# Kernel optimization log

Measured on AMD Instinct MI355X. Metric: run time of the kernel, lower is better.

Reference implementation:

```python
import jax, jax.numpy as jnp
import numpy as np

NEG = -999999.0

def setup_inputs() -> dict:
    key = jax.random.key(0)
    ks = jax.random.split(key, 8)
    B, N, H, D = 8, 2048, 1, 256  # in_dim = H*D = 256
    in_dim = H * D
    feat_in = jax.random.normal(ks[0], (B, N, in_dim), dtype=jnp.float32)
    adj = jax.random.randint(ks[1], (B, N, N), 0, 2, dtype=jnp.int32)
    # parameters (xavier-ish scales)
    W  = jax.random.normal(ks[2], (H, in_dim, D), dtype=jnp.float32) * (2.0 / (in_dim + D)) ** 0.5
    b  = jnp.zeros((D,), dtype=jnp.float32)
    Ws = jax.random.normal(ks[3], (1, 2 * D), dtype=jnp.float32) * (2.0 / (2 * D + 1)) ** 0.5  # strengh.weight
    bs = jnp.zeros((1,), dtype=jnp.float32)                                                     # strengh.bias
    Hw = jax.random.normal(ks[4], (in_dim, in_dim), dtype=jnp.float32) * (1.0 / in_dim) ** 0.5  # H.weight
    Hb = jnp.zeros((in_dim,), dtype=jnp.float32)                                                # H.bias
    return {"feat_in": feat_in, "adj": adj, "W": W, "b": b, "Ws": Ws, "bs": bs, "Hw": Hw, "Hb": Hb}

def reference(feat_in, adj, W, b, Ws, bs, Hw, Hb):
    B, N, in_dim = feat_in.shape
    H, _, D = W.shape
    h = jnp.einsum('bni,hid->bhnd', feat_in, W)                    # [B,H,N,D]
    # strengh(cat(h_src, h_dst)) decomposed: H_src[b,i,j]=h[b,i], H_dst[b,i,j]=h[b,j]
    ws_src, ws_dst = Ws[0, :D], Ws[0, D:]
    a_src = jnp.einsum('bhnd,d->bhn', h, ws_src)                   # per row i
    a_dst = jnp.einsum('bhnd,d->bhn', h, ws_dst)                   # per col j
    attn = jax.nn.sigmoid(a_src[:, :, :, None] + a_dst[:, :, None, :] + bs[0])  # [B,H,N,N]
    strict_low = jnp.tril(jnp.ones((N, N), dtype=feat_in.dtype), -1)
    attn = attn * strict_low                                        # zero outside strict lower triangle
    I_A = jnp.eye(N, dtype=feat_in.dtype) - attn                    # [B,H,N,N]
    I_A_raw = I_A
    # allowed positions: lower triangle (incl diag) AND adj==1
    low = jnp.tril(jnp.ones((N, N), dtype=jnp.bool_), 0)
    allowed = low[None, None] & (adj[:, None] == 1)                 # [B,H,N,N]
    scores = jnp.where(allowed, I_A, NEG)
    P = jax.nn.softmax(scores, axis=-1)
    feat_out = jnp.einsum('bhij,bhjd->bhid', P, h) + b              # [B,H,N,D]
    feat_out = feat_out.transpose(0, 2, 1, 3).reshape(B, N, H * D)
    feat_out = jax.nn.elu(feat_out)
    gate = jax.nn.sigmoid(feat_in @ Hw.T + Hb)
    out = gate * feat_out + (1.0 - gate) * feat_in                  # dropout = identity (eval)
    return out, I_A_raw
```

## Files before the change

kernel.cpp:

```cpp
#include <hip/hip_runtime.h>
#include <math.h>

constexpr int Bc = 8, Nc = 2048, Dc = 256;
constexpr int BN = Bc * Nc;

typedef __attribute__((ext_vector_type(8))) short short8;
typedef __attribute__((ext_vector_type(4))) float f32x4;

__device__ __forceinline__ float sigmoidf_(float x) { return 1.0f / (1.0f + expf(-x)); }

__device__ __forceinline__ unsigned short f2bf(float f) {
    unsigned int u = __float_as_uint(f);
    u = (u + 0x7FFFu + ((u >> 16) & 1u)) >> 16;
    return (unsigned short)u;
}

__device__ __forceinline__ short8 ld_frag(const unsigned short* base) {
    ushort4 lo = *(const ushort4*)(base);
    ushort4 hi = *(const ushort4*)(base + 16);
    short8 a;
    a[0] = (short)lo.x; a[1] = (short)lo.y; a[2] = (short)lo.z; a[3] = (short)lo.w;
    a[4] = (short)hi.x; a[5] = (short)hi.y; a[6] = (short)hi.z; a[7] = (short)hi.w;
    return a;
}

__device__ __forceinline__ f32x4 fz4() { f32x4 z = {0.f, 0.f, 0.f, 0.f}; return z; }

__global__ __launch_bounds__(256) void cast_kernel(const float* __restrict__ f,
                                                   unsigned short* __restrict__ o) {
    int i = (blockIdx.x * 256 + threadIdx.x) * 4;
    float4 v = *(const float4*)(f + i);
    ushort4 u = {f2bf(v.x), f2bf(v.y), f2bf(v.z), f2bf(v.w)};
    *(ushort4*)(o + i) = u;
}

__global__ __launch_bounds__(256) void pack_bt_kernel(const float* __restrict__ W,
                                                      const float* __restrict__ Hw,
                                                      unsigned short* __restrict__ BmT) {
    int idx = blockIdx.x * 256 + threadIdx.x;
    int o = idx >> 8, k = idx & 255;
    float v = (o < 256) ? W[k * 256 + o] : Hw[(o - 256) * 256 + k];
    BmT[idx] = f2bf(v);
}

__global__ __launch_bounds__(256) void gemm_mfma(const unsigned short* __restrict__ featb,
                                                 const unsigned short* __restrict__ BmT,
                                                 const float* __restrict__ Hb,
                                                 float* __restrict__ h,
                                                 float* __restrict__ gate) {
    const int tid = threadIdx.x, lane = tid & 63, w = tid >> 6;
    const int g16 = lane >> 4, li = lane & 15;
    const int m0 = blockIdx.x * 64, nw = blockIdx.y * 128 + w * 32;
    f32x4 acc[4][2];
#pragma unroll
    for (int rf = 0; rf < 4; ++rf)
#pragma unroll
        for (int cf = 0; cf < 2; ++cf) acc[rf][cf] = fz4();
    for (int k0 = 0; k0 < 256; k0 += 32) {
        short8 Af[4];
#pragma unroll
        for (int rf = 0; rf < 4; ++rf)
            Af[rf] = ld_frag(featb + (size_t)(m0 + rf * 16 + li) * 256 + k0 + g16 * 4);
#pragma unroll
        for (int cf = 0; cf < 2; ++cf) {
            short8 Bf = ld_frag(BmT + (size_t)(nw + cf * 16 + li) * 256 + k0 + g16 * 4);
#pragma unroll
            for (int rf = 0; rf < 4; ++rf)
                acc[rf][cf] = __builtin_amdgcn_mfma_f32_16x16x32_bf16(Af[rf], Bf, acc[rf][cf], 0, 0, 0);
        }
    }
#pragma unroll
    for (int rf = 0; rf < 4; ++rf)
#pragma unroll
        for (int cf = 0; cf < 2; ++cf) {
            const int n = nw + cf * 16 + li;
#pragma unroll
            for (int reg = 0; reg < 4; ++reg) {
                const int m = m0 + rf * 16 + g16 * 4 + reg;
                float v = acc[rf][cf][reg];
                if (n < 256) h[(size_t)m * 256 + n] = v;
                else gate[(size_t)m * 256 + (n - 256)] = sigmoidf_(v + Hb[n - 256]);
            }
        }
}

__global__ __launch_bounds__(256) void tr64_kernel(const float* __restrict__ h,
                                                   unsigned short* __restrict__ hT) {
    __shared__ float tile[64][65];
    const int j0 = blockIdx.x * 64, d0 = blockIdx.y * 64, b = blockIdx.z;
    const int tid = threadIdx.x;
#pragma unroll
    for (int p = 0; p < 16; ++p) {
        int idx = tid + p * 256;
        int jl = idx >> 6, dl = idx & 63;
        tile[jl][dl] = h[((size_t)b * Nc + j0 + jl) * 256 + d0 + dl];
    }
    __syncthreads();
#pragma unroll
    for (int p = 0; p < 16; ++p) {
        int idx = tid + p * 256;
        int dl = idx >> 6, jl = idx & 63;
        hT[((size_t)b * 256 + d0 + dl) * Nc + j0 + jl] = f2bf(tile[jl][dl]);
    }
}

__global__ __launch_bounds__(256) void asrc_kernel(const float* __restrict__ h,
                                                   const float* __restrict__ Ws,
                                                   float* __restrict__ a_src,
                                                   float* __restrict__ a_dst) {
    const int row = blockIdx.x * 4 + (threadIdx.x >> 6);
    const int lane = threadIdx.x & 63;
    float4 h4 = ((const float4*)(h + (size_t)row * 256))[lane];
    float4 ws = ((const float4*)Ws)[lane];
    float4 wd = ((const float4*)(Ws + 256))[lane];
    float s1 = h4.x * ws.x + h4.y * ws.y + h4.z * ws.z + h4.w * ws.w;
    float s2 = h4.x * wd.x + h4.y * wd.y + h4.z * wd.z + h4.w * wd.w;
#pragma unroll
    for (int m = 32; m >= 1; m >>= 1) {
        s1 += __shfl_xor(s1, m, 64);
        s2 += __shfl_xor(s2, m, 64);
    }
    if (lane == 0) { a_src[row] = s1; a_dst[row] = s2; }
}

__global__ __launch_bounds__(256) void mean_kernel(const float* __restrict__ h,
                                                   float* __restrict__ mean_h) {
    const int blk = blockIdx.x;
    const int b = blk >> 5, part = blk & 31;
    const int d = threadIdx.x;
    float sum = 0.f;
    const float* base = h + ((size_t)b * Nc + part * 64) * 256 + d;
#pragma unroll 4
    for (int r = 0; r < 64; ++r) sum += base[(size_t)r * 256];
    atomicAdd(&mean_h[b * 256 + d], sum);
}

constexpr int CHUNK = 8;
__global__ __launch_bounds__(256) void score_mfma(
    const int* __restrict__ adj, const unsigned short* __restrict__ hT,
    const float* __restrict__ a_src, const float* __restrict__ a_dst,
    const float* __restrict__ bs_p, float* __restrict__ out2,
    float* __restrict__ accO, float* __restrict__ sArr) {
    __shared__ unsigned short pt[32][40];
    __shared__ float sh_as[32];

    const int bid = blockIdx.x;
    const int b = bid & 7;
    int t = bid >> 3;
    int g = 0;
    while (g < 7 && 4 * (g + 1) * (g + 2) <= t) ++g;
    const int r_ = t - 4 * g * (g + 1);
    const int ib = g * 8 + r_ / (g + 1);
    const int c = r_ % (g + 1);
    const int i0 = ib * 32;
    const int t0 = c * CHUNK;
    const int t1 = min(ib + 1, t0 + CHUNK);

    const int tid = threadIdx.x;
    const int lane = tid & 63;
    const int w = tid >> 6;
    const int g16 = lane >> 4, li = lane & 15;
    const int jj_ = tid & 31;
    const int r0 = tid >> 5;
    const float bsv = bs_p[0];

    if (tid < 32) sh_as[tid] = a_src[b * Nc + i0 + tid];
    __syncthreads();

    f32x4 acc[2][4];
#pragma unroll
    for (int rf = 0; rf < 2; ++rf)
#pragma unroll
        for (int cf = 0; cf < 4; ++cf) acc[rf][cf] = fz4();
    f32x4 sacc0 = fz4(), sacc1 = fz4();
    short8 ones;
#pragma unroll
    for (int e = 0; e < 8; ++e) ones[e] = (short)0x3F80;

    const unsigned short* hTb = hT + (size_t)b * 256 * Nc;

    for (int tt = t0; tt < t1; ++tt) {
        const int j0 = tt * 32;
        if (tt > t0) __syncthreads();
        {
            const int j = j0 + jj_;
            const float adstj = a_dst[b * Nc + j];
#pragma unroll
            for (int q = 0; q < 4; ++q) {
                const int r = r0 + 8 * q;
                const int i = i0 + r;
                const int av = adj[((size_t)b * Nc + i) * Nc + j];
                float IA, p;
                if (j > i) { IA = 0.f; p = 0.f; }
                else {
                    IA = (j == i) ? 1.f : -sigmoidf_(sh_as[r] + adstj + bsv);
                    out2[((size_t)b * Nc + i) * Nc + j] = IA;
                    p = (av == 1) ? expf(IA - 1.f) : 0.f;
                }
                pt[r][jj_] = f2bf(p);
            }
        }
        __syncthreads();
        {
            short8 A0 = ld_frag(&pt[li][g16 * 4]);
            short8 A1 = ld_frag(&pt[16 + li][g16 * 4]);
            if (w == 0) {
                sacc0 = __builtin_amdgcn_mfma_f32_16x16x32_bf16(A0, ones, sacc0, 0, 0, 0);
                sacc1 = __builtin_amdgcn_mfma_f32_16x16x32_bf16(A1, ones, sacc1, 0, 0, 0);
            }
#pragma unroll
            for (int cf = 0; cf < 4; ++cf) {
                const unsigned short* bp =
                    hTb + (size_t)(w * 64 + cf * 16 + li) * Nc + j0 + g16 * 4;
                short8 Bf = ld_frag(bp);
                acc[0][cf] = __builtin_amdgcn_mfma_f32_16x16x32_bf16(A0, Bf, acc[0][cf], 0, 0, 0);
                acc[1][cf] = __builtin_amdgcn_mfma_f32_16x16x32_bf16(A1, Bf, acc[1][cf], 0, 0, 0);
            }
        }
    }
#pragma unroll
    for (int rf = 0; rf < 2; ++rf)
#pragma unroll
        for (int cf = 0; cf < 4; ++cf) {
            const int row = i0 + rf * 16 + g16 * 4;
            float* dst = accO + ((size_t)b * Nc + row) * 256 + w * 64 + cf * 16 + li;
#pragma unroll
            for (int reg = 0; reg < 4; ++reg)
                atomicAdd(dst + (size_t)reg * 256, acc[rf][cf][reg]);
        }
    if (w == 0 && li == 0) {
#pragma unroll
        for (int reg = 0; reg < 4; ++reg) {
            atomicAdd(&sArr[b * Nc + i0 + g16 * 4 + reg], sacc0[reg]);
            atomicAdd(&sArr[b * Nc + i0 + 16 + g16 * 4 + reg], sacc1[reg]);
        }
    }
}

__global__ __launch_bounds__(256) void epilogue_kernel(
    const float* __restrict__ gate, const float* __restrict__ feat,
    const float* __restrict__ bvec, const float* __restrict__ mean_h,
    const float* __restrict__ sArr, float* __restrict__ out1) {
    const int row = blockIdx.x * 4 + (threadIdx.x >> 6);
    const int lane = threadIdx.x & 63;
    const int b = row >> 11;
    const size_t g = (size_t)row * 256;
    const float s = sArr[row];
    float4 v;
    if (s == 0.f) {
        float4 mh = ((const float4*)(mean_h + b * 256))[lane];
        const float inv = 1.0f / Nc;
        v.x = mh.x * inv; v.y = mh.y * inv; v.z = mh.z * inv; v.w = mh.w * inv;
    } else {
        float4 a = ((const float4*)(out1 + g))[lane];
        const float inv = 1.0f / s;
        v.x = a.x * inv; v.y = a.y * inv; v.z = a.z * inv; v.w = a.w * inv;
    }
    const float4 b4 = ((const float4*)bvec)[lane];
    v.x += b4.x; v.y += b4.y; v.z += b4.z; v.w += b4.w;
    v.x = v.x > 0.f ? v.x : expf(v.x) - 1.f;
    v.y = v.y > 0.f ? v.y : expf(v.y) - 1.f;
    v.z = v.z > 0.f ? v.z : expf(v.z) - 1.f;
    v.w = v.w > 0.f ? v.w : expf(v.w) - 1.f;
    const float4 g4 = ((const float4*)(gate + g))[lane];
    const float4 f4 = ((const float4*)(feat + g))[lane];
    float4 o;
    o.x = g4.x * v.x + (1.f - g4.x) * f4.x;
    o.y = g4.y * v.y + (1.f - g4.y) * f4.y;
    o.z = g4.z * v.z + (1.f - g4.z) * f4.z;
    o.w = g4.w * v.w + (1.f - g4.w) * f4.w;
    ((float4*)(out1 + g))[lane] = o;
}

extern "C" void kernel_launch(void* const* d_in, const int* in_sizes, int n_in,
                              void* d_out, int out_size, void* d_ws, size_t ws_size,
                              hipStream_t stream) {
    const float* feat = (const float*)d_in[0];
    const int* adj = (const int*)d_in[1];
    const float* W = (const float*)d_in[2];
    const float* bvec = (const float*)d_in[3];
    const float* Ws = (const float*)d_in[4];
    const float* bs = (const float*)d_in[5];
    const float* Hw = (const float*)d_in[6];
    const float* Hb = (const float*)d_in[7];

    float* ws = (float*)d_ws;
    unsigned short* featb = (unsigned short*)ws;
    unsigned short* hT = featb;
    unsigned short* BmT = featb + 4194304;
    float* h = ws + 2097152 + 65536;
    float* gate = h + 4194304;
    float* a_src = gate + 4194304;
    float* a_dst = a_src + 16384;
    float* mean_h = a_dst + 16384;
    float* sArr = mean_h + 2048;

    float* out1 = (float*)d_out;
    float* out2 = out1 + (size_t)BN * 256;

    hipLaunchKernelGGL(cast_kernel, dim3(4096), dim3(256), 0, stream, feat, featb);
    hipLaunchKernelGGL(pack_bt_kernel, dim3(512), dim3(256), 0, stream, W, Hw, BmT);
    hipLaunchKernelGGL(gemm_mfma, dim3(256, 4), dim3(256), 0, stream, featb, BmT, Hb, h, gate);
    hipLaunchKernelGGL(tr64_kernel, dim3(32, 4, 8), dim3(256), 0, stream, h, hT);
    hipLaunchKernelGGL(asrc_kernel, dim3(4096), dim3(256), 0, stream, h, Ws, a_src, a_dst);
    hipMemsetAsync(mean_h, 0, 2048 * sizeof(float), stream);
    hipLaunchKernelGGL(mean_kernel, dim3(256), dim3(256), 0, stream, h, mean_h);
    hipMemsetAsync(sArr, 0, (size_t)BN * sizeof(float), stream);
    hipMemsetAsync(out1, 0, (size_t)BN * 256 * sizeof(float), stream);
    hipMemsetAsync(out2, 0, (size_t)BN * (size_t)Nc * sizeof(float), stream);
    hipLaunchKernelGGL(score_mfma, dim3(2304), dim3(256), 0, stream,
                       adj, hT, a_src, a_dst, bs, out2, out1, sArr);
    hipLaunchKernelGGL(epilogue_kernel, dim3(4096), dim3(256), 0, stream,
                       gate, feat, bvec, mean_h, sArr, out1);
}
```

Before: 454.8 us.

## Fuse score, normalization and epilogue into one per-row-block kernel

After: 494.5 us. 1.09x slower.

```diff
diff --git a/kernel.cpp b/kernel.cpp
--- a/kernel.cpp
+++ b/kernel.cpp
@@ -13,6 +13,9 @@
     unsigned int u = __float_as_uint(f);
     u = (u + 0x7FFFu + ((u >> 16) & 1u)) >> 16;
     return (unsigned short)u;
+}
+__device__ __forceinline__ float bf2f(unsigned short s) {
+    return __uint_as_float(((unsigned int)s) << 16);
 }
 
 __device__ __forceinline__ short8 ld_frag(const unsigned short* base) {
@@ -23,7 +26,6 @@
     a[4] = (short)hi.x; a[5] = (short)hi.y; a[6] = (short)hi.z; a[7] = (short)hi.w;
     return a;
 }
-
 __device__ __forceinline__ f32x4 fz4() { f32x4 z = {0.f, 0.f, 0.f, 0.f}; return z; }
 
 __global__ __launch_bounds__(256) void cast_kernel(const float* __restrict__ f,
@@ -84,8 +86,12 @@
         }
 }
 
-__global__ __launch_bounds__(256) void tr64_kernel(const float* __restrict__ h,
-                                                   unsigned short* __restrict__ hT) {
+__global__ __launch_bounds__(256) void tr64f_kernel(const float* __restrict__ h,
+                                                    const float* __restrict__ Ws,
+                                                    unsigned short* __restrict__ hT,
+                                                    float* __restrict__ a_src,
+                                                    float* __restrict__ a_dst,
+                                                    float* __restrict__ mean_h) {
     __shared__ float tile[64][65];
     const int j0 = blockIdx.x * 64, d0 = blockIdx.y * 64, b = blockIdx.z;
     const int tid = threadIdx.x;
@@ -102,174 +108,176 @@
         int dl = idx >> 6, jl = idx & 63;
         hT[((size_t)b * 256 + d0 + dl) * Nc + j0 + jl] = f2bf(tile[jl][dl]);
     }
-}
-
-__global__ __launch_bounds__(256) void asrc_kernel(const float* __restrict__ h,
-                                                   const float* __restrict__ Ws,
-                                                   float* __restrict__ a_src,
-                                                   float* __restrict__ a_dst) {
-    const int row = blockIdx.x * 4 + (threadIdx.x >> 6);
-    const int lane = threadIdx.x & 63;
-    float4 h4 = ((const float4*)(h + (size_t)row * 256))[lane];
-    float4 ws = ((const float4*)Ws)[lane];
-    float4 wd = ((const float4*)(Ws + 256))[lane];
-    float s1 = h4.x * ws.x + h4.y * ws.y + h4.z * ws.z + h4.w * ws.w;
-    float s2 = h4.x * wd.x + h4.y * wd.y + h4.z * wd.z + h4.w * wd.w;
-#pragma unroll
-    for (int m = 32; m >= 1; m >>= 1) {
-        s1 += __shfl_xor(s1, m, 64);
-        s2 += __shfl_xor(s2, m, 64);
-    }
-    if (lane == 0) { a_src[row] = s1; a_dst[row] = s2; }
-}
-
-__global__ __launch_bounds__(256) void mean_kernel(const float* __restrict__ h,
-                                                   float* __restrict__ mean_h) {
-    const int blk = blockIdx.x;
-    const int b = blk >> 5, part = blk & 31;
-    const int d = threadIdx.x;
-    float sum = 0.f;
-    const float* base = h + ((size_t)b * Nc + part * 64) * 256 + d;
-#pragma unroll 4
-    for (int r = 0; r < 64; ++r) sum += base[(size_t)r * 256];
-    atomicAdd(&mean_h[b * 256 + d], sum);
-}
-
-constexpr int CHUNK = 8;
-__global__ __launch_bounds__(256) void score_mfma(
+    {
+        const int jl = tid >> 2, q = tid & 3;
+        float s1 = 0.f, s2 = 0.f;
+#pragma unroll
+        for (int e = 0; e < 16; ++e) {
+            const float hv = tile[jl][q * 16 + e];
+            s1 = fmaf(hv, Ws[d0 + q * 16 + e], s1);
+            s2 = fmaf(hv, Ws[256 + d0 + q * 16 + e], s2);
+        }
+        s1 += __shfl_xor(s1, 1); s1 += __shfl_xor(s1, 2);
+        s2 += __shfl_xor(s2, 1); s2 += __shfl_xor(s2, 2);
+        if (q == 0) {
+            atomicAdd(&a_src[b * Nc + j0 + jl], s1);
+            atomicAdd(&a_dst[b * Nc + j0 + jl], s2);
+        }
+    }
+    {
+        const int dl = tid & 63, part = tid >> 6;
+        float sm = 0.f;
+#pragma unroll
+        for (int e = 0; e < 16; ++e) sm += tile[part * 16 + e][dl];
+        atomicAdd(&mean_h[b * 256 + d0 + dl], sm);
+    }
+}
+
+__global__ __launch_bounds__(256) void score_fused(
     const int* __restrict__ adj, const unsigned short* __restrict__ hT,
     const float* __restrict__ a_src, const float* __restrict__ a_dst,
-    const float* __restrict__ bs_p, float* __restrict__ out2,
-    float* __restrict__ accO, float* __restrict__ sArr) {
-    __shared__ unsigned short pt[32][40];
-    __shared__ float sh_as[32];
-
+    const float* __restrict__ bs_p, const float* __restrict__ bvec,
+    const float* __restrict__ gate, const float* __restrict__ feat,
+    const float* __restrict__ mean_h, float* __restrict__ out1,
+    float* __restrict__ out2) {
+    __shared__ float sh_sum[32];
     const int bid = blockIdx.x;
-    const int b = bid & 7;
-    int t = bid >> 3;
-    int g = 0;
-    while (g < 7 && 4 * (g + 1) * (g + 2) <= t) ++g;
-    const int r_ = t - 4 * g * (g + 1);
-    const int ib = g * 8 + r_ / (g + 1);
-    const int c = r_ % (g + 1);
+    const int b = bid & 7, ib = bid >> 3;
     const int i0 = ib * 32;
-    const int t0 = c * CHUNK;
-    const int t1 = min(ib + 1, t0 + CHUNK);
-
-    const int tid = threadIdx.x;
-    const int lane = tid & 63;
-    const int w = tid >> 6;
+    const int tid = threadIdx.x, lane = tid & 63, w = tid >> 6;
     const int g16 = lane >> 4, li = lane & 15;
-    const int jj_ = tid & 31;
-    const int r0 = tid >> 5;
     const float bsv = bs_p[0];
 
-    if (tid < 32) sh_as[tid] = a_src[b * Nc + i0 + tid];
+    const float as0 = a_src[b * Nc + i0 + li];
+    const float as1 = a_src[b * Nc + i0 + 16 + li];
+
+    const int* adjb = adj + (size_t)b * Nc * Nc;
+    const float* adb = a_dst + b * Nc;
+    const unsigned short* hTb = hT + (size_t)b * 256 * Nc;
+
+    f32x4 acc[2][4];
+#pragma unroll
+    for (int rf = 0; rf < 2; ++rf)
+#pragma unroll
+        for (int cf = 0; cf < 4; ++cf) acc[rf][cf] = fz4();
+    float rs0 = 0.f, rs1 = 0.f;
+
+#define LOADT(T, AJ, AD)                                                              \
+    {                                                                                 \
+        const int jq = (T) * 32;                                                      \
+        AJ[0][0] = *(const int4*)(adjb + (size_t)(i0 + li) * Nc + jq + g16 * 4);      \
+        AJ[0][1] = *(const int4*)(adjb + (size_t)(i0 + li) * Nc + jq + 16 + g16 * 4); \
+        AJ[1][0] = *(const int4*)(adjb + (size_t)(i0 + 16 + li) * Nc + jq + g16 * 4); \
+        AJ[1][1] = *(const int4*)(adjb + (size_t)(i0 + 16 + li) * Nc + jq + 16 + g16 * 4); \
+        AD[0] = *(const float4*)(adb + jq + g16 * 4);                                 \
+        AD[1] = *(const float4*)(adb + jq + 16 + g16 * 4);                            \
+    }
+
+    int4 aj[2][2]; float4 ad[2];
+    LOADT(0, aj, ad);
+    for (int t = 0; t <= ib; ++t) {
+        int4 cj[2][2] = {{aj[0][0], aj[0][1]}, {aj[1][0], aj[1][1]}};
+        float4 cd[2] = {ad[0], ad[1]};
+        if (t < ib) LOADT(t + 1, aj, ad);
+        const int j0 = t * 32;
+        short8 A[2];
+        if (t < ib) {
+#pragma unroll
+            for (int rf = 0; rf < 2; ++rf) {
+                const float asr = rf ? as1 : as0;
+                float o2[8];
+#pragma unroll
+                for (int e = 0; e < 8; ++e) {
+                    const int a_ = (e < 4) ? ((const int*)&cj[rf][0])[e] : ((const int*)&cj[rf][1])[e - 4];
+                    const float adv = (e < 4) ? ((const float*)&cd[0])[e] : ((const float*)&cd[1])[e - 4];
+                    const float IA = -sigmoidf_(asr + adv + bsv);
+                    const float p = (a_ == 1) ? expf(IA - 1.f) : 0.f;
+                    const unsigned short pb = f2bf(p);
+                    A[rf][e] = (short)pb;
+                    const float pr = bf2f(pb);
+                    if (rf == 0) rs0 += pr; else rs1 += pr;
+                    o2[e] = IA;
+                }
+                if (w == 0) {
+                    const int irow = i0 + rf * 16 + li;
+                    float4 v0 = {o2[0], o2[1], o2[2], o2[3]};
+                    float4 v1 = {o2[4], o2[5], o2[6], o2[7]};
+                    *(float4*)(out2 + ((size_t)b * Nc + irow) * Nc + j0 + g16 * 4) = v0;
+                    *(float4*)(out2 + ((size_t)b * Nc + irow) * Nc + j0 + 16 + g16 * 4) = v1;
+                }
+            }
+        } else {
+#pragma unroll
+            for (int rf = 0; rf < 2; ++rf) {
+                const int irow = i0 + rf * 16 + li;
+                const float asr = rf ? as1 : as0;
+                float o2[8];
+#pragma unroll
+                for (int e = 0; e < 8; ++e) {
+                    const int j = j0 + ((e < 4) ? (g16 * 4 + e) : (16 + g16 * 4 + e - 4));
+                    const int a_ = (e < 4) ? ((const int*)&cj[rf][0])[e] : ((const int*)&cj[rf][1])[e - 4];
+                    const float adv = (e < 4) ? ((const float*)&cd[0])[e] : ((const float*)&cd[1])[e - 4];
+                    const float IA = -sigmoidf_(asr + adv + bsv);
+                    float o2v, p;
+                    if (j > irow)       { o2v = 0.f; p = 0.f; }
+                    else if (j == irow) { o2v = 1.f; p = (a_ == 1) ? 1.f : 0.f; }
+                    else                { o2v = IA;  p = (a_ == 1) ? expf(IA - 1.f) : 0.f; }
+                    const unsigned short pb = f2bf(p);
+                    A[rf][e] = (short)pb;
+                    const float pr = bf2f(pb);
+                    if (rf == 0) rs0 += pr; else rs1 += pr;
+                    o2[e] = o2v;
+                }
+                if (w == 0) {
+                    float4 v0 = {o2[0], o2[1], o2[2], o2[3]};
+                    float4 v1 = {o2[4], o2[5], o2[6], o2[7]};
+                    *(float4*)(out2 + ((size_t)b * Nc + irow) * Nc + j0 + g16 * 4) = v0;
+                    *(float4*)(out2 + ((size_t)b * Nc + irow) * Nc + j0 + 16 + g16 * 4) = v1;
+                }
+            }
+        }
+#pragma unroll
+        for (int cf = 0; cf < 4; ++cf) {
+            short8 Bf = ld_frag(hTb + (size_t)(w * 64 + cf * 16 + li) * Nc + j0 + g16 * 4);
+            acc[0][cf] = __builtin_amdgcn_mfma_f32_16x16x32_bf16(A[0], Bf, acc[0][cf], 0, 0, 0);
+            acc[1][cf] = __builtin_amdgcn_mfma_f32_16x16x32_bf16(A[1], Bf, acc[1][cf], 0, 0, 0);
+        }
+    }
+#undef LOADT
+    rs0 += __shfl_xor(rs0, 16); rs0 += __shfl_xor(rs0, 32);
+    rs1 += __shfl_xor(rs1, 16); rs1 += __shfl_xor(rs1, 32);
+    if (w == 0 && g16 == 0) { sh_sum[li] = rs0; sh_sum[16 + li] = rs1; }
     __syncthreads();
 
-    f32x4 acc[2][4];
-#pragma unroll
-    for (int rf = 0; rf < 2; ++rf)
-#pragma unroll
-        for (int cf = 0; cf < 4; ++cf) acc[rf][cf] = fz4();
-    f32x4 sacc0 = fz4(), sacc1 = fz4();
-    short8 ones;
-#pragma unroll
-    for (int e = 0; e < 8; ++e) ones[e] = (short)0x3F80;
-
-    const unsigned short* hTb = hT + (size_t)b * 256 * Nc;
-
-    for (int tt = t0; tt < t1; ++tt) {
-        const int j0 = tt * 32;
-        if (tt > t0) __syncthreads();
-        {
-            const int j = j0 + jj_;
-            const float adstj = a_dst[b * Nc + j];
-#pragma unroll
-            for (int q = 0; q < 4; ++q) {
-                const int r = r0 + 8 * q;
-                const int i = i0 + r;
-                const int av = adj[((size_t)b * Nc + i) * Nc + j];
-                float IA, p;
-                if (j > i) { IA = 0.f; p = 0.f; }
-                else {
-                    IA = (j == i) ? 1.f : -sigmoidf_(sh_as[r] + adstj + bsv);
-                    out2[((size_t)b * Nc + i) * Nc + j] = IA;
-                    p = (av == 1) ? expf(IA - 1.f) : 0.f;
-                }
-                pt[r][jj_] = f2bf(p);
+    {
+        const float invN = 1.0f / Nc;
+#pragma unroll
+        for (int rf = 0; rf < 2; ++rf)
+#pragma unroll
+            for (int cf = 0; cf < 4; ++cf) {
+                const int col = w * 64 + cf * 16 + li;
+                const float bb = bvec[col];
+#pragma unroll
+                for (int reg = 0; reg < 4; ++reg) {
+                    const int row = i0 + rf * 16 + g16 * 4 + reg;
+                    const float s = sh_sum[rf * 16 + g16 * 4 + reg];
+                    const size_t g = ((size_t)b * Nc + row) * 256 + col;
+                    float v = (s == 0.f) ? mean_h[b * 256 + col] * invN : acc[rf][cf][reg] / s;
+                    v += bb;
+                    v = v > 0.f ? v : expf(v) - 1.f;
+                    const float gt = gate[g];
+                    out1[g] = gt * v + (1.f - gt) * feat[g];
+                }
             }
-        }
-        __syncthreads();
-        {
-            short8 A0 = ld_frag(&pt[li][g16 * 4]);
-            short8 A1 = ld_frag(&pt[16 + li][g16 * 4]);
-            if (w == 0) {
-                sacc0 = __builtin_amdgcn_mfma_f32_16x16x32_bf16(A0, ones, sacc0, 0, 0, 0);
-                sacc1 = __builtin_amdgcn_mfma_f32_16x16x32_bf16(A1, ones, sacc1, 0, 0, 0);
-            }
-#pragma unroll
-            for (int cf = 0; cf < 4; ++cf) {
-                const unsigned short* bp =
-                    hTb + (size_t)(w * 64 + cf * 16 + li) * Nc + j0 + g16 * 4;
-                short8 Bf = ld_frag(bp);
-                acc[0][cf] = __builtin_amdgcn_mfma_f32_16x16x32_bf16(A0, Bf, acc[0][cf], 0, 0, 0);
-                acc[1][cf] = __builtin_amdgcn_mfma_f32_16x16x32_bf16(A1, Bf, acc[1][cf], 0, 0, 0);
-            }
-        }
-    }
-#pragma unroll
-    for (int rf = 0; rf < 2; ++rf)
-#pragma unroll
-        for (int cf = 0; cf < 4; ++cf) {
-            const int row = i0 + rf * 16 + g16 * 4;
-            float* dst = accO + ((size_t)b * Nc + row) * 256 + w * 64 + cf * 16 + li;
-#pragma unroll
-            for (int reg = 0; reg < 4; ++reg)
-                atomicAdd(dst + (size_t)reg * 256, acc[rf][cf][reg]);
-        }
-    if (w == 0 && li == 0) {
-#pragma unroll
-        for (int reg = 0; reg < 4; ++reg) {
-            atomicAdd(&sArr[b * Nc + i0 + g16 * 4 + reg], sacc0[reg]);
-            atomicAdd(&sArr[b * Nc + i0 + 16 + g16 * 4 + reg], sacc1[reg]);
-        }
-    }
-}
-
-__global__ __launch_bounds__(256) void epilogue_kernel(
-    const float* __restrict__ gate, const float* __restrict__ feat,
-    const float* __restrict__ bvec, const float* __restrict__ mean_h,
-    const float* __restrict__ sArr, float* __restrict__ out1) {
-    const int row = blockIdx.x * 4 + (threadIdx.x >> 6);
-    const int lane = threadIdx.x & 63;
-    const int b = row >> 11;
-    const size_t g = (size_t)row * 256;
-    const float s = sArr[row];
-    float4 v;
-    if (s == 0.f) {
-        float4 mh = ((const float4*)(mean_h + b * 256))[lane];
-        const float inv = 1.0f / Nc;
-        v.x = mh.x * inv; v.y = mh.y * inv; v.z = mh.z * inv; v.w = mh.w * inv;
-    } else {
-        float4 a = ((const float4*)(out1 + g))[lane];
-        const float inv = 1.0f / s;
-        v.x = a.x * inv; v.y = a.y * inv; v.z = a.z * inv; v.w = a.w * inv;
-    }
-    const float4 b4 = ((const float4*)bvec)[lane];
-    v.x += b4.x; v.y += b4.y; v.z += b4.z; v.w += b4.w;
-    v.x = v.x > 0.f ? v.x : expf(v.x) - 1.f;
-    v.y = v.y > 0.f ? v.y : expf(v.y) - 1.f;
-    v.z = v.z > 0.f ? v.z : expf(v.z) - 1.f;
-    v.w = v.w > 0.f ? v.w : expf(v.w) - 1.f;
-    const float4 g4 = ((const float4*)(gate + g))[lane];
-    const float4 f4 = ((const float4*)(feat + g))[lane];
-    float4 o;
-    o.x = g4.x * v.x + (1.f - g4.x) * f4.x;
-    o.y = g4.y * v.y + (1.f - g4.y) * f4.y;
-    o.z = g4.z * v.z + (1.f - g4.z) * f4.z;
-    o.w = g4.w * v.w + (1.f - g4.w) * f4.w;
-    ((float4*)(out1 + g))[lane] = o;
+    }
+    {
+        const int jstart4 = (i0 + 32) >> 2;
+        const float4 z = make_float4(0.f, 0.f, 0.f, 0.f);
+        for (int r = 0; r < 32; ++r) {
+            float4* rowp = (float4*)(out2 + ((size_t)b * Nc + i0 + r) * Nc);
+            for (int j4 = jstart4 + tid; j4 < Nc / 4; j4 += 256) rowp[j4] = z;
+        }
+    }
 }
 
 extern "C" void kernel_launch(void* const* d_in, const int* in_sizes, int n_in,
@@ -293,7 +301,6 @@
     float* a_src = gate + 4194304;
     float* a_dst = a_src + 16384;
     float* mean_h = a_dst + 16384;
-    float* sArr = mean_h + 2048;
 
     float* out1 = (float*)d_out;
     float* out2 = out1 + (size_t)BN * 256;
@@ -301,15 +308,9 @@
     hipLaunchKernelGGL(cast_kernel, dim3(4096), dim3(256), 0, stream, feat, featb);
     hipLaunchKernelGGL(pack_bt_kernel, dim3(512), dim3(256), 0, stream, W, Hw, BmT);
     hipLaunchKernelGGL(gemm_mfma, dim3(256, 4), dim3(256), 0, stream, featb, BmT, Hb, h, gate);
-    hipLaunchKernelGGL(tr64_kernel, dim3(32, 4, 8), dim3(256), 0, stream, h, hT);
-    hipLaunchKernelGGL(asrc_kernel, dim3(4096), dim3(256), 0, stream, h, Ws, a_src, a_dst);
-    hipMemsetAsync(mean_h, 0, 2048 * sizeof(float), stream);
-    hipLaunchKernelGGL(mean_kernel, dim3(256), dim3(256), 0, stream, h, mean_h);
-    hipMemsetAsync(sArr, 0, (size_t)BN * sizeof(float), stream);
-    hipMemsetAsync(out1, 0, (size_t)BN * 256 * sizeof(float), stream);
-    hipMemsetAsync(out2, 0, (size_t)BN * (size_t)Nc * sizeof(float), stream);
-    hipLaunchKernelGGL(score_mfma, dim3(2304), dim3(256), 0, stream,
-                       adj, hT, a_src, a_dst, bs, out2, out1, sArr);
-    hipLaunchKernelGGL(epilogue_kernel, dim3(4096), dim3(256), 0, stream,
-                       gate, feat, bvec, mean_h, sArr, out1);
-}
+    hipMemsetAsync(a_src, 0, (16384 + 16384 + 2048) * sizeof(float), stream);
+    hipLaunchKernelGGL(tr64f_kernel, dim3(32, 4, 8), dim3(256), 0, stream,
+                       h, Ws, hT, a_src, a_dst, mean_h);
+    hipLaunchKernelGGL(score_fused, dim3(512), dim3(256), 0, stream,
+                       adj, hT, a_src, a_dst, bs, bvec, gate, feat, mean_h, out1, out2);
+}
```
